# Kernel tuning notes

Hardware: AMD Instinct MI355X
Metric: run time of the kernel (lower is better)

## Reference

```python
import jax, jax.numpy as jnp
import numpy as np

B, S, D, H = 2, 2048, 1024, 16
HD = D // H  # head_dim = 64


def setup_inputs() -> dict:
    key = jax.random.key(0)
    ks = jax.random.split(key, 5)
    scale = 1.0 / np.sqrt(D)
    return {
        "x": jax.random.normal(ks[0], (B, S, D), jnp.float32),
        "Wq": jax.random.normal(ks[1], (D, D), jnp.float32) * scale,
        "Wk": jax.random.normal(ks[2], (D, D), jnp.float32) * scale,
        "Wv": jax.random.normal(ks[3], (D, D), jnp.float32) * scale,
        "Wo": jax.random.normal(ks[4], (D, D), jnp.float32) * scale,
        "bo": jnp.zeros((D,), jnp.float32),
    }


def reference(x, Wq, Wk, Wv, Wo, bo):
    b, s, d = x.shape
    # torch nn.Linear: y = x @ W.T  (W stored [d_out, d_in])
    q = (x @ Wq.T).reshape(b, s, H, HD).transpose(0, 2, 1, 3)  # [b,h,s,hd]
    k = (x @ Wk.T).reshape(b, s, H, HD).transpose(0, 2, 1, 3)
    v = (x @ Wv.T).reshape(b, s, H, HD).transpose(0, 2, 1, 3)
    scores = jnp.einsum("bhqd,bhkd->bhqk", q, k) / jnp.sqrt(jnp.float32(HD))
    causal = jnp.triu(jnp.ones((s, s), dtype=bool), k=1)
    scores = jnp.where(causal[None, None], -jnp.inf, scores)
    attn = jax.nn.softmax(scores, axis=-1)
    ctx = jnp.einsum("bhqk,bhkd->bhqd", attn, v)
    ctx = ctx.transpose(0, 2, 1, 3).reshape(b, s, d)
    return ctx @ Wo.T + bo
```

## Files before the change

kernel.cpp:

```cpp
#include <hip/hip_runtime.h>

#define B_  2
#define S_  2048
#define D_  1024
#define H_  16
#define HD_ 64
#define M_  4096

typedef __attribute__((ext_vector_type(8))) short  short8;
typedef __attribute__((ext_vector_type(4))) float  floatx4;

__device__ __forceinline__ unsigned short f2bf(float f) {
  unsigned int u = __float_as_uint(f);
  u = (u + 0x7fffu + ((u >> 16) & 1u)) >> 16;
  return (unsigned short)u;
}

__device__ __forceinline__ void gl_lds16(const short* g, short* l) {
  __builtin_amdgcn_global_load_lds(
      (const __attribute__((address_space(1))) unsigned int*)g,
      (__attribute__((address_space(3))) unsigned int*)l, 16, 0, 0);
}

__global__ __launch_bounds__(256) void cast_kernel(
    const float* __restrict__ x,  const float* __restrict__ wq,
    const float* __restrict__ wk, const float* __restrict__ wv,
    const float* __restrict__ wo,
    short* __restrict__ xb,  short* __restrict__ wqb, short* __restrict__ wkb,
    short* __restrict__ wvb, short* __restrict__ wob) {
  const float* src; short* dst; int n8;
  switch (blockIdx.y) {
    case 0:  src = x;  dst = xb;  n8 = (M_ * D_) / 8; break;
    case 1:  src = wq; dst = wqb; n8 = (D_ * D_) / 8; break;
    case 2:  src = wk; dst = wkb; n8 = (D_ * D_) / 8; break;
    case 3:  src = wv; dst = wvb; n8 = (D_ * D_) / 8; break;
    default: src = wo; dst = wob; n8 = (D_ * D_) / 8; break;
  }
  int i = blockIdx.x * 256 + threadIdx.x;
  if (i >= n8) return;
  float4 a = ((const float4*)src)[2 * i];
  float4 b = ((const float4*)src)[2 * i + 1];
  short8 o;
  o[0] = (short)f2bf(a.x); o[1] = (short)f2bf(a.y);
  o[2] = (short)f2bf(a.z); o[3] = (short)f2bf(a.w);
  o[4] = (short)f2bf(b.x); o[5] = (short)f2bf(b.y);
  o[6] = (short)f2bf(b.z); o[7] = (short)f2bf(b.w);
  ((short8*)dst)[i] = o;
}

__global__ __launch_bounds__(256) void gemm_qkv(
    const short* __restrict__ xb,  const short* __restrict__ wqb,
    const short* __restrict__ wkb, const short* __restrict__ wvb,
    short* __restrict__ qo, short* __restrict__ ko, short* __restrict__ vto) {
  __shared__ alignas(16) short As[128 * 32];
  __shared__ alignas(16) short Bs[128 * 32];
  const int tid  = threadIdx.x;
  const int lane = tid & 63, wid = tid >> 6;
  const int quad = lane >> 4, l16 = lane & 15;
  const int bn = blockIdx.x, bm = blockIdx.y, z = blockIdx.z;
  const short* wsel = (z == 0) ? wqb : ((z == 1) ? wkb : wvb);
  const float scale = (z == 0) ? 0.125f * 1.44269504f : 1.0f;
  const int lrow = wid * 32 + (lane >> 2);
  const int lcol = (lane & 3) * 8;
  const short* ag0 = xb   + (bm * 128 + lrow) * D_ + lcol;
  const short* ag1 = ag0 + 16 * D_;
  const short* bg0 = wsel + (bn * 128 + lrow) * D_ + lcol;
  const short* bg1 = bg0 + 16 * D_;
  short* la0 = &As[(wid * 32) * 32];
  short* la1 = &As[(wid * 32 + 16) * 32];
  short* lb0 = &Bs[(wid * 32) * 32];
  short* lb1 = &Bs[(wid * 32 + 16) * 32];
  const int wm = (wid & 1) * 64, wn = (wid >> 1) * 64;
  floatx4 acc[4][4];
#pragma unroll
  for (int i = 0; i < 4; i++)
#pragma unroll
    for (int j = 0; j < 4; j++) acc[i][j] = (floatx4){0.f, 0.f, 0.f, 0.f};

  for (int k0 = 0; k0 < D_; k0 += 32) {
    __syncthreads();
    gl_lds16(ag0 + k0, la0);
    gl_lds16(ag1 + k0, la1);
    gl_lds16(bg0 + k0, lb0);
    gl_lds16(bg1 + k0, lb1);
    __syncthreads();
    short8 af[4], bf[4];
#pragma unroll
    for (int t = 0; t < 4; t++) af[t] = *(const short8*)&As[(wm + t * 16 + l16) * 32 + quad * 8];
#pragma unroll
    for (int t = 0; t < 4; t++) bf[t] = *(const short8*)&Bs[(wn + t * 16 + l16) * 32 + quad * 8];
#pragma unroll
    for (int tm = 0; tm < 4; tm++)
#pragma unroll
      for (int tn = 0; tn < 4; tn++)
        acc[tm][tn] = __builtin_amdgcn_mfma_f32_16x16x32_bf16(af[tm], bf[tn], acc[tm][tn], 0, 0, 0);
  }
#pragma unroll
  for (int tm = 0; tm < 4; tm++) {
#pragma unroll
    for (int tn = 0; tn < 4; tn++) {
      int n = bn * 128 + wn + tn * 16 + l16;
      int h = n >> 6, hd = n & 63;
#pragma unroll
      for (int r = 0; r < 4; r++) {
        int m = bm * 128 + wm + tm * 16 + quad * 4 + r;
        int b = m >> 11, s = m & 2047;
        unsigned short val = f2bf(acc[tm][tn][r] * scale);
        if (z == 2)
          vto[((b * H_ + h) * HD_ + hd) * S_ + s] = (short)val;
        else if (z == 1)
          ko[((b * H_ + h) * S_ + s) * HD_ + hd] = (short)val;
        else
          qo[((b * H_ + h) * S_ + s) * HD_ + hd] = (short)val;
      }
    }
  }
}

__global__ __launch_bounds__(256) void gemm_out(
    const short* __restrict__ cx, const short* __restrict__ wob,
    const float* __restrict__ bo, float* __restrict__ out) {
  __shared__ alignas(16) short As[128 * 32];
  __shared__ alignas(16) short Bs[128 * 32];
  const int tid  = threadIdx.x;
  const int lane = tid & 63, wid = tid >> 6;
  const int quad = lane >> 4, l16 = lane & 15;
  const int bn = blockIdx.x, bm = blockIdx.y;
  const int lrow = wid * 32 + (lane >> 2);
  const int lcol = (lane & 3) * 8;
  const short* ag0 = cx  + (bm * 128 + lrow) * D_ + lcol;
  const short* ag1 = ag0 + 16 * D_;
  const short* bg0 = wob + (bn * 128 + lrow) * D_ + lcol;
  const short* bg1 = bg0 + 16 * D_;
  short* la0 = &As[(wid * 32) * 32];
  short* la1 = &As[(wid * 32 + 16) * 32];
  short* lb0 = &Bs[(wid * 32) * 32];
  short* lb1 = &Bs[(wid * 32 + 16) * 32];
  const int wm = (wid & 1) * 64, wn = (wid >> 1) * 64;
  floatx4 acc[4][4];
#pragma unroll
  for (int i = 0; i < 4; i++)
#pragma unroll
    for (int j = 0; j < 4; j++) acc[i][j] = (floatx4){0.f, 0.f, 0.f, 0.f};

  for (int k0 = 0; k0 < D_; k0 += 32) {
    __syncthreads();
    gl_lds16(ag0 + k0, la0);
    gl_lds16(ag1 + k0, la1);
    gl_lds16(bg0 + k0, lb0);
    gl_lds16(bg1 + k0, lb1);
    __syncthreads();
    short8 af[4], bf[4];
#pragma unroll
    for (int t = 0; t < 4; t++) af[t] = *(const short8*)&As[(wm + t * 16 + l16) * 32 + quad * 8];
#pragma unroll
    for (int t = 0; t < 4; t++) bf[t] = *(const short8*)&Bs[(wn + t * 16 + l16) * 32 + quad * 8];
#pragma unroll
    for (int tm = 0; tm < 4; tm++)
#pragma unroll
      for (int tn = 0; tn < 4; tn++)
        acc[tm][tn] = __builtin_amdgcn_mfma_f32_16x16x32_bf16(af[tm], bf[tn], acc[tm][tn], 0, 0, 0);
  }
#pragma unroll
  for (int tn = 0; tn < 4; tn++) {
    int n = bn * 128 + wn + tn * 16 + l16;
    float bias = bo[n];
#pragma unroll
    for (int tm = 0; tm < 4; tm++) {
#pragma unroll
      for (int r = 0; r < 4; r++) {
        int m = bm * 128 + wm + tm * 16 + quad * 4 + r;
        out[m * D_ + n] = acc[tm][tn][r] + bias;
      }
    }
  }
}

__global__ __launch_bounds__(256) void attn_kernel(
    const short* __restrict__ qbuf, const short* __restrict__ kbuf,
    const short* __restrict__ vtbuf, short* __restrict__ ctx) {
  __shared__ alignas(16) short Ks[64][72];
  __shared__ alignas(16) short Vs[64][72];
  __shared__ alignas(16) short Ps[4][16][72];
  const int tid  = threadIdx.x;
  const int lane = tid & 63, wid = tid >> 6;
  const int quad = lane >> 4, l16 = lane & 15;
  const int bx = blockIdx.x, by = blockIdx.y;
  const int qblk = ((by >> 3) & 1) ? bx : (31 - bx);
  const int bh = by;
  const int base = bh * (S_ * HD_);
  const int q0 = qblk * 64 + wid * 16;

  short8 qf0 = *(const short8*)(qbuf + base + (q0 + l16) * HD_ + quad * 8);
  short8 qf1 = *(const short8*)(qbuf + base + (q0 + l16) * HD_ + 32 + quad * 8);

  float lsum[4];
  floatx4 o[4];
#pragma unroll
  for (int r = 0; r < 4; r++) lsum[r] = 0.f;
#pragma unroll
  for (int nt = 0; nt < 4; nt++) o[nt] = (floatx4){0.f, 0.f, 0.f, 0.f};

  const int row = tid >> 2, c8 = (tid & 3) * 16;
  const short* kg = kbuf  + base + row * HD_ + c8;
  const short* vg = vtbuf + base + row * S_  + c8;
  short8 kv0 = *(const short8*)(kg);
  short8 kv1 = *(const short8*)(kg + 8);
  short8 vv0 = *(const short8*)(vg);
  short8 vv1 = *(const short8*)(vg + 8);

  for (int kt = 0; kt <= qblk; kt++) {
    __syncthreads();
    *(short8*)&Ks[row][c8]     = kv0;
    *(short8*)&Ks[row][c8 + 8] = kv1;
    *(short8*)&Vs[row][c8]     = vv0;
    *(short8*)&Vs[row][c8 + 8] = vv1;
    __syncthreads();
    {
      const int ktn = (kt < qblk) ? kt + 1 : kt;
      const short* kgn = kg + ktn * 64 * HD_;
      const short* vgn = vg + ktn * 64;
      kv0 = *(const short8*)(kgn);
      kv1 = *(const short8*)(kgn + 8);
      vv0 = *(const short8*)(vgn);
      vv1 = *(const short8*)(vgn + 8);
    }

    floatx4 sc[4];
#pragma unroll
    for (int ct = 0; ct < 4; ct++) {
      short8 kb0 = *(const short8*)&Ks[ct * 16 + l16][quad * 8];
      short8 kb1 = *(const short8*)&Ks[ct * 16 + l16][32 + quad * 8];
      floatx4 zz = (floatx4){0.f, 0.f, 0.f, 0.f};
      zz     = __builtin_amdgcn_mfma_f32_16x16x32_bf16(qf0, kb0, zz, 0, 0, 0);
      sc[ct] = __builtin_amdgcn_mfma_f32_16x16x32_bf16(qf1, kb1, zz, 0, 0, 0);
    }
    if (kt == qblk) {
#pragma unroll
      for (int ct = 0; ct < 4; ct++)
#pragma unroll
        for (int r = 0; r < 4; r++)
          if (ct * 16 + l16 > wid * 16 + quad * 4 + r) sc[ct][r] = -INFINITY;
    }
#pragma unroll
    for (int r = 0; r < 4; r++) {
#pragma unroll
      for (int ct = 0; ct < 4; ct++) {
        float p = __builtin_amdgcn_exp2f(sc[ct][r] - 32.0f);
        lsum[r] += p;
        Ps[wid][quad * 4 + r][ct * 16 + l16] = (short)(__float_as_uint(p) >> 16);
      }
    }
#pragma unroll
    for (int ks = 0; ks < 2; ks++) {
      short8 pa = *(const short8*)&Ps[wid][l16][ks * 32 + quad * 8];
#pragma unroll
      for (int nt = 0; nt < 4; nt++) {
        short8 vb = *(const short8*)&Vs[nt * 16 + l16][ks * 32 + quad * 8];
        o[nt] = __builtin_amdgcn_mfma_f32_16x16x32_bf16(pa, vb, o[nt], 0, 0, 0);
      }
    }
  }
#pragma unroll
  for (int r = 0; r < 4; r++) {
    float ls = lsum[r];
    ls += __shfl_xor(ls, 1);
    ls += __shfl_xor(ls, 2);
    ls += __shfl_xor(ls, 4);
    ls += __shfl_xor(ls, 8);
    float linv = 1.f / ls;
    int s = q0 + quad * 4 + r;
    int rowbase = ((bh >> 4) * S_ + s) * D_ + (bh & 15) * HD_;
#pragma unroll
    for (int nt = 0; nt < 4; nt++)
      ctx[rowbase + nt * 16 + l16] = (short)f2bf(o[nt][r] * linv);
  }
}

extern "C" void kernel_launch(void* const* d_in, const int* in_sizes, int n_in,
                              void* d_out, int out_size, void* d_ws, size_t ws_size,
                              hipStream_t stream) {
  const float* x  = (const float*)d_in[0];
  const float* wq = (const float*)d_in[1];
  const float* wk = (const float*)d_in[2];
  const float* wv = (const float*)d_in[3];
  const float* wo = (const float*)d_in[4];
  const float* bo = (const float*)d_in[5];
  float* out = (float*)d_out;

  char* ws = (char*)d_ws;
  short* xb  = (short*)(ws);
  short* wqb = (short*)(ws + (8u  << 20));
  short* wkb = (short*)(ws + (10u << 20));
  short* wvb = (short*)(ws + (12u << 20));
  short* wob = (short*)(ws + (14u << 20));
  short* qb  = (short*)(ws + (16u << 20));
  short* kb  = (short*)(ws + (24u << 20));
  short* cx  = (short*)(ws + (32u << 20));
  short* vtb = (short*)(ws + (40u << 20));

  cast_kernel<<<dim3(2048, 5), 256, 0, stream>>>(x, wq, wk, wv, wo, xb, wqb, wkb, wvb, wob);
  gemm_qkv   <<<dim3(8, 32, 3), 256, 0, stream>>>(xb, wqb, wkb, wvb, qb, kb, vtb);
  attn_kernel<<<dim3(32, 32),   256, 0, stream>>>(qb, kb, vtb, cx);
  gemm_out   <<<dim3(8, 32),    256, 0, stream>>>(cx, wob, bo, out);
}
```

Baseline: 188.5 us.

## Enlarge attention query tile to 128 rows with double-buffered swizzled LDS

```diff
diff --git a/kernel.cpp b/kernel.cpp
--- a/kernel.cpp
+++ b/kernel.cpp
@@ -176,20 +176,21 @@
   }
 }
 
-__global__ __launch_bounds__(256) void attn_kernel(
+__global__ __launch_bounds__(512) void attn_kernel(
     const short* __restrict__ qbuf, const short* __restrict__ kbuf,
     const short* __restrict__ vtbuf, short* __restrict__ ctx) {
-  __shared__ alignas(16) short Ks[64][72];
-  __shared__ alignas(16) short Vs[64][72];
-  __shared__ alignas(16) short Ps[4][16][72];
+  __shared__ alignas(16) short Ks[2][64][64];
+  __shared__ alignas(16) short Vs[2][64][64];
+  __shared__ alignas(16) short Ps[8][16][64];
   const int tid  = threadIdx.x;
   const int lane = tid & 63, wid = tid >> 6;
   const int quad = lane >> 4, l16 = lane & 15;
   const int bx = blockIdx.x, by = blockIdx.y;
-  const int qblk = ((by >> 3) & 1) ? bx : (31 - bx);
+  const int qt = ((by >> 4) & 1) ? bx : (15 - bx);
   const int bh = by;
   const int base = bh * (S_ * HD_);
-  const int q0 = qblk * 64 + wid * 16;
+  const int q0 = qt * 128 + wid * 16;
+  const int NT = 2 * qt + 2;
 
   short8 qf0 = *(const short8*)(qbuf + base + (q0 + l16) * HD_ + quad * 8);
   short8 qf1 = *(const short8*)(qbuf + base + (q0 + l16) * HD_ + 32 + quad * 8);
@@ -201,65 +202,72 @@
 #pragma unroll
   for (int nt = 0; nt < 4; nt++) o[nt] = (floatx4){0.f, 0.f, 0.f, 0.f};
 
-  const int row = tid >> 2, c8 = (tid & 3) * 16;
-  const short* kg = kbuf  + base + row * HD_ + c8;
-  const short* vg = vtbuf + base + row * S_  + c8;
-  short8 kv0 = *(const short8*)(kg);
-  short8 kv1 = *(const short8*)(kg + 8);
-  short8 vv0 = *(const short8*)(vg);
-  short8 vv1 = *(const short8*)(vg + 8);
-
-  for (int kt = 0; kt <= qblk; kt++) {
-    __syncthreads();
-    *(short8*)&Ks[row][c8]     = kv0;
-    *(short8*)&Ks[row][c8 + 8] = kv1;
-    *(short8*)&Vs[row][c8]     = vv0;
-    *(short8*)&Vs[row][c8 + 8] = vv1;
-    __syncthreads();
-    {
-      const int ktn = (kt < qblk) ? kt + 1 : kt;
-      const short* kgn = kg + ktn * 64 * HD_;
-      const short* vgn = vg + ktn * 64;
-      kv0 = *(const short8*)(kgn);
-      kv1 = *(const short8*)(kgn + 8);
-      vv0 = *(const short8*)(vgn);
-      vv1 = *(const short8*)(vgn + 8);
-    }
-
-    floatx4 sc[4];
-#pragma unroll
-    for (int ct = 0; ct < 4; ct++) {
-      short8 kb0 = *(const short8*)&Ks[ct * 16 + l16][quad * 8];
-      short8 kb1 = *(const short8*)&Ks[ct * 16 + l16][32 + quad * 8];
-      floatx4 zz = (floatx4){0.f, 0.f, 0.f, 0.f};
-      zz     = __builtin_amdgcn_mfma_f32_16x16x32_bf16(qf0, kb0, zz, 0, 0, 0);
-      sc[ct] = __builtin_amdgcn_mfma_f32_16x16x32_bf16(qf1, kb1, zz, 0, 0, 0);
-    }
-    if (kt == qblk) {
-#pragma unroll
-      for (int ct = 0; ct < 4; ct++)
-#pragma unroll
-        for (int r = 0; r < 4; r++)
-          if (ct * 16 + l16 > wid * 16 + quad * 4 + r) sc[ct][r] = -INFINITY;
-    }
-#pragma unroll
-    for (int r = 0; r < 4; r++) {
+  const int srow  = tid >> 3;
+  const int sslot = tid & 7;
+  const int swz   = ((sslot ^ (srow & 7)) << 3);
+  const short* kg = kbuf  + base + srow * HD_ + sslot * 8;
+  const short* vg = vtbuf + base + srow * S_  + sslot * 8;
+
+  short8 kreg = *(const short8*)(kg);
+  short8 vreg = *(const short8*)(vg);
+  *(short8*)&Ks[0][srow][swz] = kreg;
+  *(short8*)&Vs[0][srow][swz] = vreg;
+  kreg = *(const short8*)(kg + 64 * HD_);
+  vreg = *(const short8*)(vg + 64);
+  __syncthreads();
+
+  const int x16 = l16 & 7;
+  for (int kt = 0; kt < NT; kt++) {
+    const int b = kt & 1;
+    if (kt + 1 < NT) {
+      *(short8*)&Ks[b ^ 1][srow][swz] = kreg;
+      *(short8*)&Vs[b ^ 1][srow][swz] = vreg;
+    }
+    if (kt + 2 < NT) {
+      kreg = *(const short8*)(kg + (kt + 2) * 64 * HD_);
+      vreg = *(const short8*)(vg + (kt + 2) * 64);
+    }
+    if (kt * 64 <= q0 + 15) {
+      floatx4 sc[4];
 #pragma unroll
       for (int ct = 0; ct < 4; ct++) {
-        float p = __builtin_amdgcn_exp2f(sc[ct][r] - 32.0f);
-        lsum[r] += p;
-        Ps[wid][quad * 4 + r][ct * 16 + l16] = (short)(__float_as_uint(p) >> 16);
-      }
-    }
-#pragma unroll
-    for (int ks = 0; ks < 2; ks++) {
-      short8 pa = *(const short8*)&Ps[wid][l16][ks * 32 + quad * 8];
-#pragma unroll
-      for (int nt = 0; nt < 4; nt++) {
-        short8 vb = *(const short8*)&Vs[nt * 16 + l16][ks * 32 + quad * 8];
-        o[nt] = __builtin_amdgcn_mfma_f32_16x16x32_bf16(pa, vb, o[nt], 0, 0, 0);
-      }
-    }
+        int row = ct * 16 + l16, rx = row & 7;
+        short8 kb0 = *(const short8*)&Ks[b][row][(quad ^ rx) << 3];
+        short8 kb1 = *(const short8*)&Ks[b][row][((4 + quad) ^ rx) << 3];
+        floatx4 zz = (floatx4){-32.f, -32.f, -32.f, -32.f};
+        zz     = __builtin_amdgcn_mfma_f32_16x16x32_bf16(qf0, kb0, zz, 0, 0, 0);
+        sc[ct] = __builtin_amdgcn_mfma_f32_16x16x32_bf16(qf1, kb1, zz, 0, 0, 0);
+      }
+      if (kt * 64 + 63 > q0) {
+#pragma unroll
+        for (int ct = 0; ct < 4; ct++)
+#pragma unroll
+          for (int r = 0; r < 4; r++)
+            if (kt * 64 + ct * 16 + l16 > q0 + quad * 4 + r) sc[ct][r] = -INFINITY;
+      }
+#pragma unroll
+      for (int r = 0; r < 4; r++) {
+        int prow = quad * 4 + r, px = prow & 7;
+#pragma unroll
+        for (int ct = 0; ct < 4; ct++) {
+          float p = __builtin_amdgcn_exp2f(sc[ct][r]);
+          lsum[r] += p;
+          int cslot = ct * 2 + (l16 >> 3);
+          Ps[wid][prow][((cslot ^ px) << 3) + x16] = (short)(__float_as_uint(p) >> 16);
+        }
+      }
+#pragma unroll
+      for (int ks = 0; ks < 2; ks++) {
+        short8 pa = *(const short8*)&Ps[wid][l16][((ks * 4 + quad) ^ x16) << 3];
+#pragma unroll
+        for (int nt = 0; nt < 4; nt++) {
+          int vrow = nt * 16 + l16;
+          short8 vb = *(const short8*)&Vs[b][vrow][((ks * 4 + quad) ^ (vrow & 7)) << 3];
+          o[nt] = __builtin_amdgcn_mfma_f32_16x16x32_bf16(pa, vb, o[nt], 0, 0, 0);
+        }
+      }
+    }
+    __syncthreads();
   }
 #pragma unroll
   for (int r = 0; r < 4; r++) {
@@ -301,6 +309,6 @@
 
   cast_kernel<<<dim3(2048, 5), 256, 0, stream>>>(x, wq, wk, wv, wo, xb, wqb, wkb, wvb, wob);
   gemm_qkv   <<<dim3(8, 32, 3), 256, 0, stream>>>(xb, wqb, wkb, wvb, qb, kb, vtb);
-  attn_kernel<<<dim3(32, 32),   256, 0, stream>>>(qb, kb, vtb, cx);
+  attn_kernel<<<dim3(16, 32),   512, 0, stream>>>(qb, kb, vtb, cx);
   gemm_out   <<<dim3(8, 32),    256, 0, stream>>>(cx, wob, bo, out);
 }
```

New measurement: 179.0 us. 5.0% less time.
